# Kernel tuning notes

Measured on AMD Instinct MI355X. Metric: run time of the kernel, lower is better.

Reference implementation:

```python
import jax, jax.numpy as jnp
import numpy as np

N = 65536   # total goals in library
D = 256     # flattened embedding dim
B = 2048    # batch_size (last B entries are the new batch)


def setup_inputs() -> dict:
    key = jax.random.key(0)
    k1, k2 = jax.random.split(key)
    return {
        "target_lib": jax.random.normal(k1, (N, D), dtype=jnp.float32),
        "reached_lib": jax.random.normal(k2, (N, D), dtype=jnp.float32),
        "batch_size": B,
    }


def _euclid(a, b):
    # distance_fn: Euclidean distance between two embeddings
    return jnp.sqrt(jnp.sum((a - b) ** 2))


def _nearest_idx(queries, lib):
    # top-1 nearest neighbor via squared-distance expansion (same argmin as cdist)
    qn = jnp.sum(queries * queries, axis=1, keepdims=True)      # [B,1]
    ln = jnp.sum(lib * lib, axis=1)                             # [L]
    d2 = qn + ln[None, :] - 2.0 * (queries @ lib.T)             # [B,L]
    return jnp.argmin(d2, axis=1)                               # [B]


def reference(target_lib, reached_lib, batch_size):
    targets = target_lib[-batch_size:]          # [B,D] newest target goals
    reached = reached_lib[-batch_size:]         # [B,D] newest reached goals
    prev = reached_lib[:-batch_size]            # [N-B,D] previously reached goals

    prev_closest = prev[_nearest_idx(targets, prev)]       # [B,D]
    new_closest = reached[_nearest_idx(targets, reached)]  # [B,D]

    def LP(t, init_e, reached_e):
        return _euclid(t, init_e) - _euclid(t, reached_e)

    IM_vals, IM_grads = jax.vmap(jax.value_and_grad(LP, 0))(
        targets, prev_closest, new_closest)
    return IM_vals, IM_grads
```

## Files before the change

### kernel.cpp

```cpp
#include <hip/hip_runtime.h>
#include <math.h>

#define NTOT   65536
#define DDIM   256
#define BATCH  2048
#define NPREV  (NTOT - BATCH)

#define PWP    32
#define PWR    32
#define UPC_P  31
#define UPC_R  1
#define BNC_P  31
#define BNC_R  16

#define INF_F 3.402823466e+38f
#define SWZ(r) ((((r) & 3)) ^ ((((r) >> 2) & 3)))

typedef float  f32x4  __attribute__((ext_vector_type(4)));
typedef float  f32x16 __attribute__((ext_vector_type(16)));
typedef _Float16 half8 __attribute__((ext_vector_type(8)));

#define TILE_HALVES 65536

#define SCHED_FENCE() __builtin_amdgcn_sched_barrier(0)
#define RAW_BARRIER() do { SCHED_FENCE(); __builtin_amdgcn_s_barrier(); SCHED_FENCE(); } while (0)
#define VMCNT4()  do { asm volatile("s_waitcnt vmcnt(4)" ::: "memory"); SCHED_FENCE(); } while (0)
#define VMCNT0()  do { asm volatile("s_waitcnt vmcnt(0)" ::: "memory"); SCHED_FENCE(); } while (0)
#define LGKM0()   do { asm volatile("s_waitcnt lgkmcnt(0)" ::: "memory"); SCHED_FENCE(); } while (0)
#define NOVM()    do { } while (0)

__global__ void lp_norms(const float* __restrict__ lib, float* __restrict__ ln) {
    const int row  = blockIdx.x * 4 + (threadIdx.x >> 6);
    const int lane = threadIdx.x & 63;
    const float4 v = reinterpret_cast<const float4*>(lib + (size_t)row * DDIM)[lane];
    float s = v.x * v.x + v.y * v.y + v.z * v.z + v.w * v.w;
#pragma unroll
    for (int off = 32; off > 0; off >>= 1) s += __shfl_down(s, off);
    if (lane == 0) ln[row] = s;
}

__device__ __forceinline__ void cvt_split(const f32x4 a, const f32x4 b,
                                          half8& h, half8& l) {
    float v[8] = {a[0], a[1], a[2], a[3], b[0], b[1], b[2], b[3]};
#pragma unroll
    for (int j = 0; j < 8; ++j) {
        const float s = v[j] * 256.0f;
        const _Float16 hh = (_Float16)s;
        const _Float16 ll = (_Float16)(s - (float)hh);
        h[j] = hh; l[j] = ll;
    }
}

__global__ void lp_split32_all(const float* __restrict__ reached,
                               const float* __restrict__ Qp,
                               _Float16* __restrict__ Lsp, _Float16* __restrict__ Qsp,
                               float* __restrict__ ln) {
    const int b    = blockIdx.x;
    const int t    = threadIdx.x;
    const int rg   = t >> 6;
    const int l    = t & 63;
    const int row  = rg * 32 + (l & 31);
    const int k8   = l >> 5;

    const float* srcT;
    _Float16*    dstT;
    float*       lnT;
    int          lnBase = 0;
    if (b < NTOT / 128) {
        srcT = reached + (size_t)b * 128 * DDIM;
        dstT = Lsp + (size_t)b * TILE_HALVES;
        lnT  = ln; lnBase = b * 128;
    } else {
        const int qt = b - NTOT / 128;
        srcT = Qp + (size_t)qt * 128 * DDIM;
        dstT = Qsp + (size_t)qt * TILE_HALVES;
        lnT  = nullptr;
    }
    const float* srcR = srcT + (size_t)row * DDIM;

    float nsum = 0.f;
#pragma unroll
    for (int kb = 0; kb < 8; ++kb) {
#pragma unroll
        for (int kk = 0; kk < 2; ++kk) {
            const float* p = srcR + kb * 32 + kk * 16 + k8 * 8;
            const f32x4 a = *reinterpret_cast<const f32x4*>(p);
            const f32x4 bb = *reinterpret_cast<const f32x4*>(p + 4);
            half8 h, lo; cvt_split(a, bb, h, lo);
            const size_t off = ((size_t)(((kb * 2 + 0) * 4 + rg) * 2 + kk) * 64 + l) * 8;
            *reinterpret_cast<half8*>(dstT + off)        = h;
            *reinterpret_cast<half8*>(dstT + off + 4096) = lo;
            nsum += a[0]*a[0] + a[1]*a[1] + a[2]*a[2] + a[3]*a[3]
                  + bb[0]*bb[0] + bb[1]*bb[1] + bb[2]*bb[2] + bb[3]*bb[3];
        }
    }
    nsum += __shfl_xor(nsum, 32);
    if (lnT != nullptr && k8 == 0) lnT[(size_t)lnBase + row] = nsum;
}

__device__ __forceinline__ void gload16(const _Float16* g, _Float16* lds) {
    __builtin_amdgcn_global_load_lds(
        (const __attribute__((address_space(1))) void*)g,
        (__attribute__((address_space(3))) void*)lds, 16, 0, 0);
}

#define READ8(R, BASE)                                                           \
    _Pragma("unroll")                                                            \
    for (int nf = 0; nf < 2; ++nf)                                               \
      _Pragma("unroll")                                                          \
      for (int hl = 0; hl < 2; ++hl)                                             \
        _Pragma("unroll")                                                        \
        for (int kk = 0; kk < 2; ++kk)                                           \
          R[nf][hl][kk] = *reinterpret_cast<const half8*>(                       \
              (BASE) + hl * 2048 + nf * 1024 + kk * 512 + lane * 8);

#define MFMA12(kb_, RC)                                                          \
    _Pragma("unroll")                                                            \
    for (int kk = 0; kk < 2; ++kk)                                               \
      _Pragma("unroll")                                                          \
      for (int term = 0; term < 3; ++term) {                                     \
        const int ta = (term == 2) ? 1 : 0;                                      \
        const int tb = (term == 1) ? 1 : 0;                                      \
        acc[0] = __builtin_amdgcn_mfma_f32_32x32x16_f16(                         \
            qf[kb_][ta][kk], RC[0][tb][kk], acc[0], 0, 0, 0);                    \
        acc[1] = __builtin_amdgcn_mfma_f32_32x32x16_f16(                         \
            qf[kb_][ta][kk], RC[1][tb][kk], acc[1], 0, 0, 0);                    \
      }

#define NN_PAIR(j_, STAGE_OK, ENDVM, READE_OK, FOLD_OK)                          \
  {                                                                              \
    const int p_ = un * 4 + (j_);                                                \
    VMCNT4();                                                                    \
    RAW_BARRIER();                                                               \
    LGKM0();                        \
    __builtin_amdgcn_s_setprio(1);                                               \
    MFMA12(2 * (j_), bfE)                                                        \
    __builtin_amdgcn_s_setprio(0);                                               \
    { const _Float16* Bc = &LB[p_ % 3][4096]; READ8(bfO, Bc) }                    \
    LGKM0();                                                                     \
    if (STAGE_OK) stageP((p_ + 2) % 3, p_ + 2);                                  \
    __builtin_amdgcn_s_setprio(1);                                               \
    MFMA12(2 * (j_) + 1, bfO)                                                    \
    __builtin_amdgcn_s_setprio(0);                                               \
    ENDVM;                                                                       \
    if (READE_OK) { const _Float16* Bn = &LB[(p_ + 1) % 3][0]; READ8(bfE, Bn) }   \
    if (FOLD_OK) fold(un);                                                       \
  }

__global__ __launch_bounds__(256, 2)
void lp_nn_mfma12(const _Float16* __restrict__ Qs, const _Float16* __restrict__ Ls,
                  const float* __restrict__ ln, int unitsPC, int nchunks,
                  float* __restrict__ pscore, int* __restrict__ pidx)
{
    __shared__ _Float16 LB[3][8192];
    __shared__ float lnLds[2048];

    const int nwg  = 16 * nchunks;
    const int hid  = blockIdx.x;
    const int work = (hid & 7) * (nwg >> 3) + (hid >> 3);
    const int bx   = work & 15;
    const int by   = work >> 4;

    const int t    = threadIdx.x;
    const int lane = t & 63;
    const int wid  = t >> 6;
    const int col  = lane & 31, hi = lane >> 5;

    const _Float16* Qt = Qs + (size_t)bx * TILE_HALVES;
    const int u0 = by * unitsPC;

    half8 qf[8][2][2];
#pragma unroll
    for (int kb = 0; kb < 8; ++kb)
#pragma unroll
        for (int hl = 0; hl < 2; ++hl)
#pragma unroll
            for (int kk = 0; kk < 2; ++kk)
                qf[kb][hl][kk] = *reinterpret_cast<const half8*>(
                    Qt + ((((kb * 2 + hl) * 4 + wid) * 2) + kk) * 512 + lane * 8);

    auto stageP = [&](int buf, int p) {
        const int u = u0 + (p >> 2), kb0 = (p & 3) * 2;
        const int tile = u >> 1, half = u & 1;
        const _Float16* base = Ls + (size_t)tile * TILE_HALVES;
#pragma unroll
        for (int dkb = 0; dkb < 2; ++dkb)
#pragma unroll
            for (int hl = 0; hl < 2; ++hl)
                gload16(base + (((kb0 + dkb) * 2 + hl) * 4 + half * 2) * 1024 + t * 8,
                        &LB[buf][(dkb * 2 + hl) * 2048 + wid * 512]);
    };

    float bkey[16];
    int   bidxr[16];
    f32x16 acc[2];
#pragma unroll
    for (int r = 0; r < 16; ++r) { bkey[r] = INF_F; bidxr[r] = 0x7fffffff; }
    acc[0] = (f32x16)(0.f); acc[1] = (f32x16)(0.f);

    auto fold = [&](int un) {
        const int u = u0 + un;
        const float lnv0 = lnLds[un * 64 + col];
        const float lnv1 = lnLds[un * 64 + 32 + col];
#pragma unroll
        for (int nf = 0; nf < 2; ++nf) {
            const int gidx = u * 64 + nf * 32 + col;
            const float lnvs = (nf ? lnv1 : lnv0) * 65536.0f;
#pragma unroll
            for (int r = 0; r < 16; ++r) {
                const float key = fmaf(-2.f, acc[nf][r], lnvs);
                if (key < bkey[r] || (key == bkey[r] && gidx < bidxr[r])) {
                    bkey[r] = key; bidxr[r] = gidx;
                }
                acc[nf][r] = 0.f;
            }
        }
    };

    {
        const float* lsrc = ln + (size_t)u0 * 64;
#pragma unroll
        for (int j = 0; j < 2; ++j)
            __builtin_amdgcn_global_load_lds(
                (const __attribute__((address_space(1))) void*)(lsrc + j * 1024 + t * 4),
                (__attribute__((address_space(3))) void*)(&lnLds[j * 1024 + wid * 256]),
                16, 0, 0);
    }
    stageP(0, 0);
    stageP(1, 1);
    VMCNT4();
    RAW_BARRIER();

    half8 bfE[2][2][2], bfO[2][2][2];
    { const _Float16* B0 = &LB[0][0]; READ8(bfE, B0) }

    for (int un = 0; un < unitsPC - 1; ++un) {
        NN_PAIR(0, true, VMCNT4(), true, false)
        NN_PAIR(1, true, VMCNT4(), true, false)
        NN_PAIR(2, true, VMCNT4(), true, false)
        NN_PAIR(3, true, VMCNT4(), true, true)
    }
    {
        const int un = unitsPC - 1;
        NN_PAIR(0, true,  VMCNT4(), true,  false)
        NN_PAIR(1, true,  VMCNT4(), true,  false)
        NN_PAIR(2, false, VMCNT0(), true,  false)
        NN_PAIR(3, false, NOVM(),   false, true)
    }

#pragma unroll
    for (int off = 1; off < 32; off <<= 1)
#pragma unroll
        for (int r = 0; r < 16; ++r) {
            const float ok = __shfl_xor(bkey[r], off);
            const int   oi = __shfl_xor(bidxr[r], off);
            if (ok < bkey[r] || (ok == bkey[r] && oi < bidxr[r])) {
                bkey[r] = ok; bidxr[r] = oi;
            }
        }
    if (col == 0)
#pragma unroll
        for (int r = 0; r < 16; ++r) {
            const int q = bx * 128 + wid * 32 + (r & 3) + 8 * (r >> 2) + 4 * hi;
            pscore[(size_t)q * nchunks + by] = bkey[r];
            pidx  [(size_t)q * nchunks + by] = bidxr[r];
        }
}

__global__ __launch_bounds__(256, 2)
void lp_nn_mfma_fb(const float* __restrict__ Q, const float* __restrict__ L,
                   const float* __restrict__ ln, int chunkRows,
                   float* __restrict__ pscore, int* __restrict__ pidx, int nchunks)
{
    __shared__ _Float16 Ah[128 * 32];
    __shared__ _Float16 Al[128 * 32];
    __shared__ _Float16 Bh[128 * 32];
    __shared__ _Float16 Bl[128 * 32];
    __shared__ float xk[2][128];
    __shared__ int   xi[2][128];

    const int t    = threadIdx.x;
    const int wid  = t >> 6, lane = t & 63;
    const int wq   = wid >> 1, wl = wid & 1;
    const int col  = lane & 15, rg = lane >> 4;
    const int qbase = blockIdx.x * 128;
    const int chunkBase = blockIdx.y * chunkRows;
    const int srow   = t >> 2;
    const int schunk = t & 3;

    float bkey[4][4];
    int   bidxr[4][4];
#pragma unroll
    for (int mf = 0; mf < 4; ++mf)
#pragma unroll
        for (int i = 0; i < 4; ++i) { bkey[mf][i] = INF_F; bidxr[mf][i] = 0x7fffffff; }

    for (int lt = 0; lt < chunkRows; lt += 128) {
        f32x4 acc[4][4];
#pragma unroll
        for (int mf = 0; mf < 4; ++mf)
#pragma unroll
            for (int nf = 0; nf < 4; ++nf) acc[mf][nf] = (f32x4)(0.f);

        for (int kb = 0; kb < DDIM; kb += 32) {
            __syncthreads();
#pragma unroll
            for (int sr = 0; sr < 2; ++sr) {
                const int r = srow + 64 * sr;
                const int s = schunk ^ SWZ(r);
                {
                    const float* src = Q + (size_t)(qbase + r) * DDIM + kb + schunk * 8;
                    const f32x4 a = *reinterpret_cast<const f32x4*>(src);
                    const f32x4 b = *reinterpret_cast<const f32x4*>(src + 4);
                    half8 h, l; cvt_split(a, b, h, l);
                    *reinterpret_cast<half8*>(&Ah[r * 32 + s * 8]) = h;
                    *reinterpret_cast<half8*>(&Al[r * 32 + s * 8]) = l;
                }
                {
                    const float* src = L + (size_t)(chunkBase + lt + r) * DDIM + kb + schunk * 8;
                    const f32x4 a = *reinterpret_cast<const f32x4*>(src);
                    const f32x4 b = *reinterpret_cast<const f32x4*>(src + 4);
                    half8 h, l; cvt_split(a, b, h, l);
                    *reinterpret_cast<half8*>(&Bh[r * 32 + s * 8]) = h;
                    *reinterpret_cast<half8*>(&Bl[r * 32 + s * 8]) = l;
                }
            }
            __syncthreads();

            half8 ah[4], al[4];
#pragma unroll
            for (int mf = 0; mf < 4; ++mf) {
                const int r = wq * 64 + mf * 16 + col;
                const int s = rg ^ SWZ(r);
                ah[mf] = *reinterpret_cast<const half8*>(&Ah[r * 32 + s * 8]);
                al[mf] = *reinterpret_cast<const half8*>(&Al[r * 32 + s * 8]);
            }
#pragma unroll
            for (int nf = 0; nf < 4; ++nf) {
                const int r = wl * 64 + nf * 16 + col;
                const int s = rg ^ SWZ(r);
                const half8 bh = *reinterpret_cast<const half8*>(&Bh[r * 32 + s * 8]);
                const half8 bl = *reinterpret_cast<const half8*>(&Bl[r * 32 + s * 8]);
#pragma unroll
                for (int mf = 0; mf < 4; ++mf) {
                    acc[mf][nf] = __builtin_amdgcn_mfma_f32_16x16x32_f16(ah[mf], bh, acc[mf][nf], 0, 0, 0);
                    acc[mf][nf] = __builtin_amdgcn_mfma_f32_16x16x32_f16(ah[mf], bl, acc[mf][nf], 0, 0, 0);
                    acc[mf][nf] = __builtin_amdgcn_mfma_f32_16x16x32_f16(al[mf], bh, acc[mf][nf], 0, 0, 0);
                }
            }
        }

#pragma unroll
        for (int nf = 0; nf < 4; ++nf) {
            const int gidx = chunkBase + lt + wl * 64 + nf * 16 + col;
            const float lnv = ln[gidx] * 65536.0f;
#pragma unroll
            for (int mf = 0; mf < 4; ++mf)
#pragma unroll
                for (int i = 0; i < 4; ++i) {
                    const float key = fmaf(-2.f, acc[mf][nf][i], lnv);
                    if (key < bkey[mf][i] || (key == bkey[mf][i] && gidx < bidxr[mf][i])) {
                        bkey[mf][i] = key; bidxr[mf][i] = gidx;
                    }
                }
        }
    }

#pragma unroll
    for (int off = 1; off < 16; off <<= 1)
#pragma unroll
        for (int mf = 0; mf < 4; ++mf)
#pragma unroll
            for (int i = 0; i < 4; ++i) {
                const float ok = __shfl_xor(bkey[mf][i], off);
                const int   oi = __shfl_xor(bidxr[mf][i], off);
                if (ok < bkey[mf][i] || (ok == bkey[mf][i] && oi < bidxr[mf][i])) {
                    bkey[mf][i] = ok; bidxr[mf][i] = oi;
                }
            }
    if (col == 0)
#pragma unroll
        for (int mf = 0; mf < 4; ++mf)
#pragma unroll
            for (int i = 0; i < 4; ++i) {
                const int ql = wq * 64 + mf * 16 + rg * 4 + i;
                xk[wl][ql] = bkey[mf][i];
                xi[wl][ql] = bidxr[mf][i];
            }
    __syncthreads();
    if (t < 128) {
        float bk = xk[0][t]; int bi = xi[0][t];
        const float k2 = xk[1][t]; const int i2 = xi[1][t];
        if (k2 < bk || (k2 == bk && i2 < bi)) { bk = k2; bi = i2; }
        const int q = qbase + t;
        pscore[(size_t)q * nchunks + blockIdx.y] = bk;
        pidx  [(size_t)q * nchunks + blockIdx.y] = bi;
    }
}

__global__ void lp_finalize(const float* __restrict__ Q,
                            const float* __restrict__ prevL,
                            const float* __restrict__ reachL,
                            const float* __restrict__ ps_p, const int* __restrict__ pi_p,
                            const float* __restrict__ ps_r, const int* __restrict__ pi_r,
                            int ncp, int ncr,
                            float* __restrict__ out)
{
    const int q = blockIdx.x;
    const int lane = threadIdx.x;

    float k1 = (lane < ncp) ? ps_p[(size_t)q * ncp + lane] : INF_F;
    int   i1 = (lane < ncp) ? pi_p[(size_t)q * ncp + lane] : 0x7fffffff;
#pragma unroll
    for (int off = 32; off > 0; off >>= 1) {
        const float ok = __shfl_xor(k1, off);
        const int   oi = __shfl_xor(i1, off);
        if (ok < k1 || (ok == k1 && oi < i1)) { k1 = ok; i1 = oi; }
    }
    float k2 = (lane < ncr) ? ps_r[(size_t)q * ncr + lane] : INF_F;
    int   i2 = (lane < ncr) ? pi_r[(size_t)q * ncr + lane] : 0x7fffffff;
#pragma unroll
    for (int off = 32; off > 0; off >>= 1) {
        const float ok = __shfl_xor(k2, off);
        const int   oi = __shfl_xor(i2, off);
        if (ok < k2 || (ok == k2 && oi < i2)) { k2 = ok; i2 = oi; }
    }

    const float4 tv = reinterpret_cast<const float4*>(Q      + (size_t)q  * DDIM)[lane];
    const float4 e1 = reinterpret_cast<const float4*>(prevL  + (size_t)i1 * DDIM)[lane];
    const float4 e2 = reinterpret_cast<const float4*>(reachL + (size_t)i2 * DDIM)[lane];
    const float4 d1 = {tv.x - e1.x, tv.y - e1.y, tv.z - e1.z, tv.w - e1.w};
    const float4 d2 = {tv.x - e2.x, tv.y - e2.y, tv.z - e2.z, tv.w - e2.w};
    float s1 = d1.x * d1.x + d1.y * d1.y + d1.z * d1.z + d1.w * d1.w;
    float s2 = d2.x * d2.x + d2.y * d2.y + d2.z * d2.z + d2.w * d2.w;
#pragma unroll
    for (int off = 32; off > 0; off >>= 1) {
        s1 += __shfl_xor(s1, off);
        s2 += __shfl_xor(s2, off);
    }
    const float r1 = sqrtf(s1), r2 = sqrtf(s2);
    float4 g;
    g.x = d1.x / r1 - d2.x / r2;
    g.y = d1.y / r1 - d2.y / r2;
    g.z = d1.z / r1 - d2.z / r2;
    g.w = d1.w / r1 - d2.w / r2;
    reinterpret_cast<float4*>(out + BATCH + (size_t)q * DDIM)[lane] = g;
    if (lane == 0) out[q] = r1 - r2;
}

extern "C" void kernel_launch(void* const* d_in, const int* in_sizes, int n_in,
                              void* d_out, int out_size, void* d_ws, size_t ws_size,
                              hipStream_t stream) {
    const float* target_lib  = (const float*)d_in[0];
    const float* reached_lib = (const float*)d_in[1];
    const float* Qp     = target_lib  + (size_t)NPREV * DDIM;
    const float* prevL  = reached_lib;
    const float* reachL = reached_lib + (size_t)NPREV * DDIM;

    float* ws     = (float*)d_ws;
    float* ln_all = ws;
    float* ps_p   = ln_all + NTOT;
    float* ps_r   = ps_p + (size_t)BATCH * PWP;
    int*   pi_p   = (int*)(ps_r + (size_t)BATCH * PWR);
    int*   pi_r   = pi_p + (size_t)BATCH * PWP;
    _Float16* Qsp = (_Float16*)(pi_r + (size_t)BATCH * PWR);
    _Float16* Lsp = Qsp + (size_t)(BATCH / 128) * TILE_HALVES;
    float* out    = (float*)d_out;

    const size_t need = (size_t)(NTOT + 2 * BATCH * (PWP + PWR)) * 4
                      + (size_t)(BATCH / 128 + NTOT / 128) * TILE_HALVES * 2;

    if (ws_size >= need) {
        lp_split32_all<<<NTOT / 128 + BATCH / 128, 256, 0, stream>>>(
            reached_lib, Qp, Lsp, Qsp, ln_all);
        lp_nn_mfma12<<<16 * PWP, 256, 0, stream>>>(
            Qsp, Lsp, ln_all, UPC_P, PWP, ps_p, pi_p);
        lp_nn_mfma12<<<16 * PWR, 256, 0, stream>>>(
            Qsp, Lsp + (size_t)(NPREV / 128) * TILE_HALVES,
            ln_all + NPREV, UPC_R, PWR, ps_r, pi_r);
        lp_finalize<<<BATCH, 64, 0, stream>>>(
            Qp, prevL, reachL, ps_p, pi_p, ps_r, pi_r, PWP, PWR, out);
    } else {
        lp_norms<<<NTOT / 4, 256, 0, stream>>>(reached_lib, ln_all);
        lp_nn_mfma_fb<<<dim3(BATCH / 128, BNC_P), 256, 0, stream>>>(
            Qp, prevL, ln_all, 2048, ps_p, pi_p, BNC_P);
        lp_nn_mfma_fb<<<dim3(BATCH / 128, BNC_R), 256, 0, stream>>>(
            Qp, reachL, ln_all + NPREV, 128, ps_r, pi_r, BNC_R);
        lp_finalize<<<BATCH, 64, 0, stream>>>(
            Qp, prevL, reachL, ps_p, pi_p, ps_r, pi_r, BNC_P, BNC_R, out);
    }
}
```

Before: 237.6 us.

## Load library tiles straight from global into registers, dropping LDS triple-buffering

Replaces the LDS triple-buffered global_load_lds pipeline, with its explicit waitcnt and barriers, by direct per-wave global loads of the library fragments into registers inside the main loop. The per-unit norm values are read from global memory instead of LDS. This removes the workgroup barriers and LDS traffic, but each wave now loads B fragments independently and relies on the compiler and cache for latency hiding, with no explicit prefetch.

```diff
diff --git a/kernel.cpp b/kernel.cpp
--- a/kernel.cpp
+++ b/kernel.cpp
@@ -21,13 +21,6 @@
 typedef _Float16 half8 __attribute__((ext_vector_type(8)));
 
 #define TILE_HALVES 65536
-
-#define SCHED_FENCE() __builtin_amdgcn_sched_barrier(0)
-#define RAW_BARRIER() do { SCHED_FENCE(); __builtin_amdgcn_s_barrier(); SCHED_FENCE(); } while (0)
-#define VMCNT4()  do { asm volatile("s_waitcnt vmcnt(4)" ::: "memory"); SCHED_FENCE(); } while (0)
-#define VMCNT0()  do { asm volatile("s_waitcnt vmcnt(0)" ::: "memory"); SCHED_FENCE(); } while (0)
-#define LGKM0()   do { asm volatile("s_waitcnt lgkmcnt(0)" ::: "memory"); SCHED_FENCE(); } while (0)
-#define NOVM()    do { } while (0)
 
 __global__ void lp_norms(const float* __restrict__ lib, float* __restrict__ ln) {
     const int row  = blockIdx.x * 4 + (threadIdx.x >> 6);
@@ -98,22 +91,6 @@
     if (lnT != nullptr && k8 == 0) lnT[(size_t)lnBase + row] = nsum;
 }
 
-__device__ __forceinline__ void gload16(const _Float16* g, _Float16* lds) {
-    __builtin_amdgcn_global_load_lds(
-        (const __attribute__((address_space(1))) void*)g,
-        (__attribute__((address_space(3))) void*)lds, 16, 0, 0);
-}
-
-#define READ8(R, BASE)                                                           \
-    _Pragma("unroll")                                                            \
-    for (int nf = 0; nf < 2; ++nf)                                               \
-      _Pragma("unroll")                                                          \
-      for (int hl = 0; hl < 2; ++hl)                                             \
-        _Pragma("unroll")                                                        \
-        for (int kk = 0; kk < 2; ++kk)                                           \
-          R[nf][hl][kk] = *reinterpret_cast<const half8*>(                       \
-              (BASE) + hl * 2048 + nf * 1024 + kk * 512 + lane * 8);
-
 #define MFMA12(kb_, RC)                                                          \
     _Pragma("unroll")                                                            \
     for (int kk = 0; kk < 2; ++kk)                                               \
@@ -127,34 +104,11 @@
             qf[kb_][ta][kk], RC[1][tb][kk], acc[1], 0, 0, 0);                    \
       }
 
-#define NN_PAIR(j_, STAGE_OK, ENDVM, READE_OK, FOLD_OK)                          \
-  {                                                                              \
-    const int p_ = un * 4 + (j_);                                                \
-    VMCNT4();                                                                    \
-    RAW_BARRIER();                                                               \
-    LGKM0();                        \
-    __builtin_amdgcn_s_setprio(1);                                               \
-    MFMA12(2 * (j_), bfE)                                                        \
-    __builtin_amdgcn_s_setprio(0);                                               \
-    { const _Float16* Bc = &LB[p_ % 3][4096]; READ8(bfO, Bc) }                    \
-    LGKM0();                                                                     \
-    if (STAGE_OK) stageP((p_ + 2) % 3, p_ + 2);                                  \
-    __builtin_amdgcn_s_setprio(1);                                               \
-    MFMA12(2 * (j_) + 1, bfO)                                                    \
-    __builtin_amdgcn_s_setprio(0);                                               \
-    ENDVM;                                                                       \
-    if (READE_OK) { const _Float16* Bn = &LB[(p_ + 1) % 3][0]; READ8(bfE, Bn) }   \
-    if (FOLD_OK) fold(un);                                                       \
-  }
-
 __global__ __launch_bounds__(256, 2)
-void lp_nn_mfma12(const _Float16* __restrict__ Qs, const _Float16* __restrict__ Ls,
-                  const float* __restrict__ ln, int unitsPC, int nchunks,
-                  float* __restrict__ pscore, int* __restrict__ pidx)
+void lp_nn_reg(const _Float16* __restrict__ Qs, const _Float16* __restrict__ Ls,
+               const float* __restrict__ ln, int unitsPC, int nchunks,
+               float* __restrict__ pscore, int* __restrict__ pidx)
 {
-    __shared__ _Float16 LB[3][8192];
-    __shared__ float lnLds[2048];
-
     const int nwg  = 16 * nchunks;
     const int hid  = blockIdx.x;
     const int work = (hid & 7) * (nwg >> 3) + (hid >> 3);
@@ -179,18 +133,6 @@
                 qf[kb][hl][kk] = *reinterpret_cast<const half8*>(
                     Qt + ((((kb * 2 + hl) * 4 + wid) * 2) + kk) * 512 + lane * 8);
 
-    auto stageP = [&](int buf, int p) {
-        const int u = u0 + (p >> 2), kb0 = (p & 3) * 2;
-        const int tile = u >> 1, half = u & 1;
-        const _Float16* base = Ls + (size_t)tile * TILE_HALVES;
-#pragma unroll
-        for (int dkb = 0; dkb < 2; ++dkb)
-#pragma unroll
-            for (int hl = 0; hl < 2; ++hl)
-                gload16(base + (((kb0 + dkb) * 2 + hl) * 4 + half * 2) * 1024 + t * 8,
-                        &LB[buf][(dkb * 2 + hl) * 2048 + wid * 512]);
-    };
-
     float bkey[16];
     int   bidxr[16];
     f32x16 acc[2];
@@ -198,10 +140,28 @@
     for (int r = 0; r < 16; ++r) { bkey[r] = INF_F; bidxr[r] = 0x7fffffff; }
     acc[0] = (f32x16)(0.f); acc[1] = (f32x16)(0.f);
 
-    auto fold = [&](int un) {
+    for (int un = 0; un < unitsPC; ++un) {
         const int u = u0 + un;
-        const float lnv0 = lnLds[un * 64 + col];
-        const float lnv1 = lnLds[un * 64 + 32 + col];
+        const _Float16* Bu = Ls + (size_t)(u >> 1) * TILE_HALVES + (size_t)(u & 1) * 2048;
+        const float lnv0 = ln[u * 64 + col];
+        const float lnv1 = ln[u * 64 + 32 + col];
+
+#pragma unroll
+        for (int kb = 0; kb < 8; ++kb) {
+            half8 bf[2][2][2];
+#pragma unroll
+            for (int nf = 0; nf < 2; ++nf)
+#pragma unroll
+                for (int hl = 0; hl < 2; ++hl)
+#pragma unroll
+                    for (int kk = 0; kk < 2; ++kk)
+                        bf[nf][hl][kk] = *reinterpret_cast<const half8*>(
+                            Bu + (size_t)(((kb * 2 + hl) * 4 + nf) * 1024 + kk * 512 + lane * 8));
+            __builtin_amdgcn_s_setprio(1);
+            MFMA12(kb, bf)
+            __builtin_amdgcn_s_setprio(0);
+        }
+
 #pragma unroll
         for (int nf = 0; nf < 2; ++nf) {
             const int gidx = u * 64 + nf * 32 + col;
@@ -215,37 +175,6 @@
                 acc[nf][r] = 0.f;
             }
         }
-    };
-
-    {
-        const float* lsrc = ln + (size_t)u0 * 64;
-#pragma unroll
-        for (int j = 0; j < 2; ++j)
-            __builtin_amdgcn_global_load_lds(
-                (const __attribute__((address_space(1))) void*)(lsrc + j * 1024 + t * 4),
-                (__attribute__((address_space(3))) void*)(&lnLds[j * 1024 + wid * 256]),
-                16, 0, 0);
-    }
-    stageP(0, 0);
-    stageP(1, 1);
-    VMCNT4();
-    RAW_BARRIER();
-
-    half8 bfE[2][2][2], bfO[2][2][2];
-    { const _Float16* B0 = &LB[0][0]; READ8(bfE, B0) }
-
-    for (int un = 0; un < unitsPC - 1; ++un) {
-        NN_PAIR(0, true, VMCNT4(), true, false)
-        NN_PAIR(1, true, VMCNT4(), true, false)
-        NN_PAIR(2, true, VMCNT4(), true, false)
-        NN_PAIR(3, true, VMCNT4(), true, true)
-    }
-    {
-        const int un = unitsPC - 1;
-        NN_PAIR(0, true,  VMCNT4(), true,  false)
-        NN_PAIR(1, true,  VMCNT4(), true,  false)
-        NN_PAIR(2, false, VMCNT0(), true,  false)
-        NN_PAIR(3, false, NOVM(),   false, true)
     }
 
 #pragma unroll
@@ -473,9 +402,9 @@
     if (ws_size >= need) {
         lp_split32_all<<<NTOT / 128 + BATCH / 128, 256, 0, stream>>>(
             reached_lib, Qp, Lsp, Qsp, ln_all);
-        lp_nn_mfma12<<<16 * PWP, 256, 0, stream>>>(
+        lp_nn_reg<<<16 * PWP, 256, 0, stream>>>(
             Qsp, Lsp, ln_all, UPC_P, PWP, ps_p, pi_p);
-        lp_nn_mfma12<<<16 * PWR, 256, 0, stream>>>(
+        lp_nn_reg<<<16 * PWR, 256, 0, stream>>>(
             Qsp, Lsp + (size_t)(NPREV / 128) * TILE_HALVES,
             ln_all + NPREV, UPC_R, PWR, ps_r, pi_r);
         lp_finalize<<<BATCH, 64, 0, stream>>>(
```

Result: slower. 264.2 us (+11.2%).
